# Kernel optimization log

Measured on AMD Instinct MI355X. Metric: run time of the kernel, lower is better.

## Reference

```python
import jax, jax.numpy as jnp
import numpy as np
import math

N_HEAD = 16
ROPE_BASE = 10000.0


def _rope_cos_sin(seq_len, head_dim, dtype):
    # standard RoPE tables: freqs_i = base^(-2i/d), i in [0, d/2)
    half = head_dim // 2
    inv_freq = ROPE_BASE ** (-(jnp.arange(half, dtype=jnp.float32) * 2.0 / head_dim))
    t = jnp.arange(seq_len, dtype=jnp.float32)
    ang = t[:, None] * inv_freq[None, :]  # [S, d/2]
    return jnp.cos(ang).astype(dtype), jnp.sin(ang).astype(dtype)


def _apply_rope(x, cos, sin):
    # x: [B, S, H, d]; rotate interleaved even/odd pairs
    x1 = x[..., 0::2]
    x2 = x[..., 1::2]
    c = cos[None, :, None, :]
    s = sin[None, :, None, :]
    out = jnp.stack([x1 * c - x2 * s, x1 * s + x2 * c], axis=-1)
    return out.reshape(x.shape)


def setup_inputs() -> dict:
    key = jax.random.key(0)
    kx, kq, kk, kv, ko = jax.random.split(key, 5)
    B, S, H = 2, 2048, 1024
    x = jax.random.normal(kx, (B, S, H), dtype=jnp.float32)
    scale = 0.02
    w_q = jax.random.normal(kq, (H, H), dtype=jnp.float32) * scale
    w_k = jax.random.normal(kk, (H, H), dtype=jnp.float32) * scale
    w_v = jax.random.normal(kv, (H, H), dtype=jnp.float32) * scale
    w_o = jax.random.normal(ko, (H, H), dtype=jnp.float32) * scale
    return {"x": x, "w_q": w_q, "w_k": w_k, "w_v": w_v, "w_o": w_o}


def reference(x, w_q, w_k, w_v, w_o):
    B, S, H = x.shape
    d = H // N_HEAD
    # torch nn.Linear(bias=False): y = x @ W^T, W is [out, in]
    q = (x @ w_q.T).reshape(B, S, N_HEAD, d)
    k = (x @ w_k.T).reshape(B, S, N_HEAD, d)
    v = (x @ w_v.T).reshape(B, S, N_HEAD, d)
    cos, sin = _rope_cos_sin(S, d, x.dtype)
    q = _apply_rope(q, cos, sin)
    k = _apply_rope(k, cos, sin)
    scores = jnp.einsum("bqhd,bkhd->bhqk", q, k) / math.sqrt(d)
    coefs = jax.nn.softmax(scores, axis=-1)
    # NOTE: causal mask is applied AFTER softmax via tril (no renormalization)
    causal = jnp.tril(jnp.ones((S, S), dtype=bool))
    coefs = jnp.where(causal[None, None], coefs, 0.0)
    out = jnp.einsum("bhqk,bkhd->bqhd", coefs, v).reshape(B, S, H)
    return out @ w_o.T
```

## Files before the change

kernel.cpp:

```cpp
#include <hip/hip_runtime.h>
#include <math.h>

#define SEQ   2048
#define HDIM  1024
#define NH    16
#define DH    64
#define MTOT  4096
#define BHTOT 32

typedef _Float16 half_t;
typedef __attribute__((ext_vector_type(2))) __fp16 fp16x2;
typedef __attribute__((ext_vector_type(4))) _Float16 half4;
typedef __attribute__((ext_vector_type(8))) _Float16 half8;
typedef __attribute__((ext_vector_type(4))) float float4v;

typedef __attribute__((address_space(1))) const unsigned int guint;
typedef __attribute__((address_space(3))) unsigned int luint;
__device__ __forceinline__ void glds16(const half_t* g, half_t* l) {
    __builtin_amdgcn_global_load_lds((guint*)g, (luint*)l, 16, 0, 0);
}

__global__ __launch_bounds__(256)
void prep(const float* __restrict__ x,  const float* __restrict__ wq,
          const float* __restrict__ wk, const float* __restrict__ wv,
          const float* __restrict__ wo,
          half_t* __restrict__ xh,  half_t* __restrict__ wqh,
          half_t* __restrict__ wkh, half_t* __restrict__ wvh,
          half_t* __restrict__ woh, float2* __restrict__ rope)
{
    const int bid = blockIdx.x;
    if (bid < 8192) {
        int i = bid * 256 + threadIdx.x;
        const float* s; half_t* d;
        if (i < 1048576) { s = x; d = xh; }
        else {
            int j = i - 1048576;
            int w = j >> 18; i = j & 262143;
            s = (w == 0) ? wq : (w == 1) ? wk : (w == 2) ? wv : wo;
            d = (w == 0) ? wqh : (w == 1) ? wkh : (w == 2) ? wvh : woh;
        }
        float4 v = ((const float4*)s)[i];
        union { half_t h[4]; uint2 u; } tmp;
        tmp.h[0] = (half_t)v.x; tmp.h[1] = (half_t)v.y;
        tmp.h[2] = (half_t)v.z; tmp.h[3] = (half_t)v.w;
        ((uint2*)d)[i] = tmp.u;
    } else {
        int tt = (bid - 8192) * 256 + threadIdx.x;
        int s = tt >> 5, j = tt & 31;
        float inv = powf(10000.0f, -(float)j / 32.0f);
        float ang = (float)s * inv;
        rope[tt] = make_float2(cosf(ang), sinf(ang));
    }
}

__global__ __launch_bounds__(256, 5)
void gemm_qkv(const half_t* __restrict__ A,
              const half_t* __restrict__ w0, const half_t* __restrict__ w1,
              const half_t* __restrict__ w2,
              half_t* __restrict__ Qb, half_t* __restrict__ Kb,
              half_t* __restrict__ Vtb,
              const float2* __restrict__ rope)
{
    const int mode = blockIdx.z;
    const half_t* Bw = (mode == 1) ? w1 : (mode == 2) ? w2 : w0;

    __shared__ __align__(16) half_t Tsh[2][128][64];
    half_t (*Ash)[64] = Tsh[0];
    half_t (*Bsh)[64] = Tsh[1];

    const int t    = threadIdx.x;
    const int lane = t & 63;
    const int wave = t >> 6;
    const int quad = lane >> 4;
    const int l16  = lane & 15;
    const int wr   = (wave >> 1) * 64;
    const int wc   = (wave & 1) * 64;
    const int bm   = blockIdx.x, bn = blockIdx.y;

    const int srow   = lane >> 3;
    const int schunk = (lane & 7) ^ (srow & 3);
    const half_t* Asrc = A  + (size_t)(bm * 128 + srow) * HDIM + schunk * 8;
    const half_t* Bsrc = Bw + (size_t)(bn * 128 + srow) * HDIM + schunk * 8;
    const int swz = (l16 & 3) << 4;

    float4v acc[4][4] = {};

    for (int kt = 0; kt < HDIM / 64; ++kt) {
        const half_t* Ak = Asrc + kt * 64;
        const half_t* Bk = Bsrc + kt * 64;
#pragma unroll
        for (int c = 0; c < 4; ++c) {
            const int r8 = wave * 32 + c * 8;
            glds16(Ak + (size_t)r8 * HDIM, &Ash[r8][0]);
            glds16(Bk + (size_t)r8 * HDIM, &Bsh[r8][0]);
        }
        __syncthreads();
#pragma unroll
        for (int kk = 0; kk < 2; ++kk) {
            const int cb = ((quad << 4) | (kk << 6)) ^ swz;
            half8 af[4], bf[4];
#pragma unroll
            for (int mb = 0; mb < 4; ++mb)
                af[mb] = *(const half8*)((const char*)&Ash[wr + mb * 16 + l16][0] + cb);
#pragma unroll
            for (int nb = 0; nb < 4; ++nb)
                bf[nb] = *(const half8*)((const char*)&Bsh[wc + nb * 16 + l16][0] + cb);
#pragma unroll
            for (int mb = 0; mb < 4; ++mb)
#pragma unroll
                for (int nb = 0; nb < 4; ++nb)
                    acc[mb][nb] = __builtin_amdgcn_mfma_f32_16x16x32_f16(af[mb], bf[nb], acc[mb][nb], 0, 0, 0);
        }
        __syncthreads();
    }

    if (mode == 2) {
#pragma unroll
        for (int mb = 0; mb < 4; ++mb)
#pragma unroll
            for (int nb = 0; nb < 4; ++nb) {
                int row0 = bm * 128 + wr + mb * 16 + quad * 4;
                int col  = bn * 128 + wc + nb * 16 + l16;
                int b = row0 >> 11, s0 = row0 & 2047;
                int h = col >> 6,  dd = col & 63;
                union { half_t h4[4]; uint2 u; } tmp;
#pragma unroll
                for (int r = 0; r < 4; ++r) tmp.h4[r] = (half_t)acc[mb][nb][r];
                *(uint2*)&Vtb[((size_t)((b * NH + h) * DH + dd)) * SEQ + s0] = tmp.u;
            }
        return;
    }
    {
        half_t* Ob = (mode == 0) ? Qb : Kb;
        const float scl = (mode == 0) ? 0.125f * 1.44269504088896f : 1.0f;
        const int h = (bn * 128 + wc) >> 6;
        float* E = (float*)&Tsh[0][0][0] + wave * 1088;
#pragma unroll
        for (int mb = 0; mb < 4; ++mb) {
#pragma unroll
            for (int nb = 0; nb < 4; ++nb)
#pragma unroll
                for (int r = 0; r < 4; ++r)
                    E[(quad * 4 + r) * 68 + nb * 16 + l16] = acc[mb][nb][r];
            __asm__ volatile("s_waitcnt lgkmcnt(0)" ::: "memory");
#pragma unroll
            for (int c = 0; c < 2; ++c) {
                const int uidx = c * 64 + lane;
                const int row = uidx >> 3, ch = uidx & 7;
                const int sg = bm * 128 + wr + mb * 16 + row;
                const int b = sg >> 11, s = sg & 2047;
                const float* Er = E + row * 68 + ch * 8;
                const float4 e0 = *(const float4*)Er;
                const float4 e1 = *(const float4*)(Er + 4);
                const float4* rp = (const float4*)(rope + (size_t)s * 32 + ch * 4);
                const float4 r01 = rp[0];
                const float4 r23 = rp[1];
                union { half_t hh[8]; uint4 u; } o;
                o.hh[0] = (half_t)((e0.x * r01.x - e0.y * r01.y) * scl);
                o.hh[1] = (half_t)((e0.x * r01.y + e0.y * r01.x) * scl);
                o.hh[2] = (half_t)((e0.z * r01.z - e0.w * r01.w) * scl);
                o.hh[3] = (half_t)((e0.z * r01.w + e0.w * r01.z) * scl);
                o.hh[4] = (half_t)((e1.x * r23.x - e1.y * r23.y) * scl);
                o.hh[5] = (half_t)((e1.x * r23.y + e1.y * r23.x) * scl);
                o.hh[6] = (half_t)((e1.z * r23.z - e1.w * r23.w) * scl);
                o.hh[7] = (half_t)((e1.z * r23.w + e1.w * r23.z) * scl);
                *(uint4*)&Ob[((size_t)((b * NH + h) * SEQ + s)) * DH + ch * 8] = o.u;
            }
        }
    }
}

__global__ __launch_bounds__(256)
void gemm_out(const half_t* __restrict__ A, const half_t* __restrict__ W,
              float* __restrict__ outF)
{
    __shared__ __align__(16) half_t Ash[2][64][64];
    __shared__ __align__(16) half_t Bsh[2][64][64];

    const int t    = threadIdx.x;
    const int lane = t & 63;
    const int wave = t >> 6;
    const int quad = lane >> 4;
    const int l16  = lane & 15;
    const int wr   = (wave >> 1) * 32;
    const int wc   = (wave & 1) * 32;
    const int bm   = blockIdx.x, bn = blockIdx.y;

    const int srow   = lane >> 3;
    const int schunk = (lane & 7) ^ (srow & 3);
    const half_t* Asrc = A + (size_t)(bm * 64 + srow) * HDIM + schunk * 8;
    const half_t* Bsrc = W + (size_t)(bn * 64 + srow) * HDIM + schunk * 8;
    const int swz = (l16 & 3) << 4;

    auto stage = [&](int kt, int buf) {
        const half_t* Ak = Asrc + kt * 64;
        const half_t* Bk = Bsrc + kt * 64;
#pragma unroll
        for (int c = 0; c < 2; ++c) {
            const int r8 = wave * 16 + c * 8;
            glds16(Ak + (size_t)r8 * HDIM, &Ash[buf][r8][0]);
            glds16(Bk + (size_t)r8 * HDIM, &Bsh[buf][r8][0]);
        }
    };

    float4v acc[2][2] = {};

    stage(0, 0);
    __asm__ volatile("s_waitcnt vmcnt(0)" ::: "memory");
    __builtin_amdgcn_s_barrier();
    __builtin_amdgcn_sched_barrier(0);

    for (int kt = 0; kt < HDIM / 64; ++kt) {
        const int cur = kt & 1, nxt = cur ^ 1;
        if (kt + 1 < HDIM / 64) stage(kt + 1, nxt);
#pragma unroll
        for (int kk = 0; kk < 2; ++kk) {
            const int cb = ((quad << 4) | (kk << 6)) ^ swz;
            half8 af[2], bf[2];
#pragma unroll
            for (int mb = 0; mb < 2; ++mb)
                af[mb] = *(const half8*)((const char*)&Ash[cur][wr + mb * 16 + l16][0] + cb);
#pragma unroll
            for (int nb = 0; nb < 2; ++nb)
                bf[nb] = *(const half8*)((const char*)&Bsh[cur][wc + nb * 16 + l16][0] + cb);
#pragma unroll
            for (int mb = 0; mb < 2; ++mb)
#pragma unroll
                for (int nb = 0; nb < 2; ++nb)
                    acc[mb][nb] = __builtin_amdgcn_mfma_f32_16x16x32_f16(af[mb], bf[nb], acc[mb][nb], 0, 0, 0);
        }
        __asm__ volatile("s_waitcnt vmcnt(0)" ::: "memory");
        __builtin_amdgcn_s_barrier();
        __builtin_amdgcn_sched_barrier(0);
    }

#pragma unroll
    for (int mb = 0; mb < 2; ++mb)
#pragma unroll
        for (int nb = 0; nb < 2; ++nb) {
            int row0 = bm * 64 + wr + mb * 16 + quad * 4;
            int col  = bn * 64 + wc + nb * 16 + l16;
#pragma unroll
            for (int r = 0; r < 4; ++r)
                outF[(size_t)(row0 + r) * HDIM + col] = acc[mb][nb][r];
        }
}

__global__ __launch_bounds__(512, 4)
void attn_fused(const half_t* __restrict__ Qb, const half_t* __restrict__ Kb,
                const half_t* __restrict__ Vtb, half_t* __restrict__ AOut)
{
    const int bx = blockIdx.x;
    const int p  = bx >> 1;
    const int hf = bx & 1;
    const int bh = blockIdx.y;
    const int NT = SEQ / 128;

    __shared__ __align__(16) half_t Ksh[2][128][64];
    __shared__ __align__(16) half_t Vsh[2][64][128];

    const int t = threadIdx.x;
    const int wave = t >> 6, lane = t & 63, quad = lane >> 4, l16 = lane & 15;
    const int heavy = wave >> 2, wl = wave & 3;
    const int qtile = heavy ? (15 - p) : p;
    const int q0 = qtile * 128 + hf * 64 + wl * 16;
    const int vtop = 15 - p;

    const half_t* Qp = Qb + ((size_t)bh * SEQ + q0 + l16) * DH + quad * 8;
    const half8 qf0 = *(const half8*)Qp;
    const half8 qf1 = *(const half8*)(Qp + 32);

    float4v o[4] = {};
    float4v ls = {};

    const int krow = lane >> 3, kpos = lane & 7;
    const int kchunk = kpos ^ krow;
    const half_t* Ksrc = Kb + ((size_t)bh * SEQ + wave * 16 + krow) * DH + kchunk * 8;
    const int ko1 = ((quad ^ (l16 & 7)) * 8);
    const int ko2 = ko1 ^ 32;

    const int sr  = t >> 3;
    const int sc0 = t & 7;
    const half_t* Vg = Vtb + ((size_t)bh * DH + sr) * SEQ + sc0 * 8;
    const int vso0 = ((sc0    ) ^ (sr & 15)) * 8;
    const int vso1 = ((sc0 + 8) ^ (sr & 15)) * 8;

    {
        uint4 va0 = *(const uint4*)(Vg);
        uint4 va1 = *(const uint4*)(Vg + 64);
        glds16(Ksrc,          &Ksh[0][wave * 16][0]);
        glds16(Ksrc + 8 * DH, &Ksh[0][wave * 16 + 8][0]);
        *(uint4*)&Vsh[0][sr][vso0] = va0;
        *(uint4*)&Vsh[0][sr][vso1] = va1;
    }
    __asm__ volatile("s_waitcnt vmcnt(0)" ::: "memory");
    __asm__ volatile("s_waitcnt lgkmcnt(0)" ::: "memory");
    __builtin_amdgcn_s_barrier();
    __builtin_amdgcn_sched_barrier(0);

    for (int T = 0; T < NT; ++T) {
        const int cur = T & 1, nxt = cur ^ 1;
        const bool kn = (T + 1 < NT);
        const bool vn = kn && (T + 1 <= vtop);

        uint4 va0, va1;
        if (vn) {
            va0 = *(const uint4*)(Vg + (T + 1) * 128);
            va1 = *(const uint4*)(Vg + (T + 1) * 128 + 64);
        }
        if (kn) {
            const half_t* Kn = Ksrc + (size_t)(T + 1) * 128 * DH;
            glds16(Kn,          &Ksh[nxt][wave * 16][0]);
            glds16(Kn + 8 * DH, &Ksh[nxt][wave * 16 + 8][0]);
        }

#pragma unroll
        for (int hh = 0; hh < 2; ++hh) {
            float4v sc[4];
            __builtin_amdgcn_s_setprio(1);
#pragma unroll
            for (int nb = 0; nb < 4; ++nb) {
                const half_t* kp = &Ksh[cur][hh * 64 + nb * 16 + l16][0];
                half8 kf0 = *(const half8*)(kp + ko1);
                half8 kf1 = *(const half8*)(kp + ko2);
                float4v a = {};
                a = __builtin_amdgcn_mfma_f32_16x16x32_f16(kf0, qf0, a, 0, 0, 0);
                a = __builtin_amdgcn_mfma_f32_16x16x32_f16(kf1, qf1, a, 0, 0, 0);
                sc[nb] = a;
            }
            __builtin_amdgcn_s_setprio(0);

#pragma unroll
            for (int nb = 0; nb < 4; ++nb)
#pragma unroll
                for (int r = 0; r < 4; ++r) {
                    float e = __builtin_amdgcn_exp2f(sc[nb][r]);
                    sc[nb][r] = e;
                    ls[r] += e;
                }

            const int kbase = T * 128 + hh * 64;
            if (kbase <= q0 + 15) {
                if (kbase + 63 > q0) {
                    int qg = q0 + l16;
#pragma unroll
                    for (int nb = 0; nb < 4; ++nb)
#pragma unroll
                        for (int r = 0; r < 4; ++r)
                            if (kbase + nb * 16 + quad * 4 + r > qg) sc[nb][r] = 0.f;
                }
                half4 pf[4];
#pragma unroll
                for (int nb = 0; nb < 4; ++nb) {
                    union { fp16x2 v2[2]; half4 v4; } u;
                    u.v2[0] = __builtin_amdgcn_cvt_pkrtz(sc[nb][0], sc[nb][1]);
                    u.v2[1] = __builtin_amdgcn_cvt_pkrtz(sc[nb][2], sc[nb][3]);
                    pf[nb] = u.v4;
                }
                __builtin_amdgcn_s_setprio(1);
#pragma unroll
                for (int md = 0; md < 4; ++md) {
                    const char* vrow = (const char*)&Vsh[cur][md * 16 + l16][0];
#pragma unroll
                    for (int nb = 0; nb < 4; ++nb) {
                        const int chunk = (hh * 8 + nb * 2 + (quad >> 1)) ^ l16;
                        half4 vf = *(const half4*)(vrow + chunk * 16 + (quad & 1) * 8);
                        o[md] = __builtin_amdgcn_mfma_f32_16x16x16f16(vf, pf[nb], o[md], 0, 0, 0);
                    }
                }
                __builtin_amdgcn_s_setprio(0);
            }
        }

        if (vn) {
            *(uint4*)&Vsh[nxt][sr][vso0] = va0;
            *(uint4*)&Vsh[nxt][sr][vso1] = va1;
        }
        __asm__ volatile("s_waitcnt vmcnt(0)" ::: "memory");
        __asm__ volatile("s_waitcnt lgkmcnt(0)" ::: "memory");
        __builtin_amdgcn_s_barrier();
        __builtin_amdgcn_sched_barrier(0);
    }

    const int b = bh >> 4, h = bh & 15;
    const int orow = lane >> 2, occ = (lane & 3) * 16;
    half_t* scr = (heavy ? (half_t*)Vsh : (half_t*)Ksh) + wl * 1152;
    half_t (*Osh)[72] = (half_t(*)[72])scr;
    {
        float rs = (ls[0] + ls[1]) + (ls[2] + ls[3]);
        rs += __shfl_xor(rs, 16, 64);
        rs += __shfl_xor(rs, 32, 64);
        const float inv = 1.0f / rs;
#pragma unroll
        for (int md = 0; md < 4; ++md)
#pragma unroll
            for (int r = 0; r < 4; ++r)
                Osh[l16][md * 16 + quad * 4 + r] = (half_t)(o[md][r] * inv);
        __asm__ volatile("s_waitcnt lgkmcnt(0)" ::: "memory");
        uint4 o0 = *(const uint4*)&Osh[orow][occ];
        uint4 o1 = *(const uint4*)&Osh[orow][occ + 8];
        const int s = q0 + orow;
        half_t* dst = AOut + ((size_t)(b * SEQ + s)) * HDIM + h * DH + occ;
        *(uint4*)dst       = o0;
        *(uint4*)(dst + 8) = o1;
    }
}

extern "C" void kernel_launch(void* const* d_in, const int* in_sizes, int n_in,
                              void* d_out, int out_size, void* d_ws, size_t ws_size,
                              hipStream_t stream)
{
    const float* x  = (const float*)d_in[0];
    const float* wq = (const float*)d_in[1];
    const float* wk = (const float*)d_in[2];
    const float* wv = (const float*)d_in[3];
    const float* wo = (const float*)d_in[4];
    float* out = (float*)d_out;

    char* ws = (char*)d_ws;
    size_t off = 0;
    auto alloc = [&](size_t bytes) -> void* {
        void* p = ws + off;
        off += (bytes + 255) & ~(size_t)255;
        return p;
    };
    half_t* xh   = (half_t*)alloc((size_t)MTOT * HDIM * 2);
    half_t* wqh  = (half_t*)alloc((size_t)HDIM * HDIM * 2);
    half_t* wkh  = (half_t*)alloc((size_t)HDIM * HDIM * 2);
    half_t* wvh  = (half_t*)alloc((size_t)HDIM * HDIM * 2);
    half_t* woh  = (half_t*)alloc((size_t)HDIM * HDIM * 2);
    half_t* Qb   = (half_t*)alloc((size_t)BHTOT * SEQ * DH * 2);
    half_t* Kb   = (half_t*)alloc((size_t)BHTOT * SEQ * DH * 2);
    half_t* Vtb  = (half_t*)alloc((size_t)BHTOT * SEQ * DH * 2);
    half_t* ah   = (half_t*)alloc((size_t)MTOT * HDIM * 2);
    float2* rope = (float2*)alloc((size_t)SEQ * 32 * sizeof(float2));

    prep<<<8448, 256, 0, stream>>>(x, wq, wk, wv, wo, xh, wqh, wkh, wvh, woh, rope);

    gemm_qkv<<<dim3(32, 8, 3), 256, 0, stream>>>(xh, wqh, wkh, wvh,
                                                 Qb, Kb, Vtb, rope);
    attn_fused<<<dim3(16, 32), 512, 0, stream>>>(Qb, Kb, Vtb, ah);
    gemm_out<<<dim3(64, 16), 256, 0, stream>>>(ah, woh, out);
}
```

Measured before the change: 186.6 us.

## Process paired light and heavy query tiles per wave to reuse K/V fragments

Each wave now handles two 16-row query groups (one from tile p and one from tile 15-p) instead of one, so every K and V fragment read from shared memory feeds two MFMA chains. The grid is halved to 8x32 blocks with each block covering a full 128-row tile pair, and the launch bounds drop to 2 blocks per SM to leave room for the doubled accumulators. The aim is to cut LDS traffic per MFMA and raise the share of time spent on matrix math. In exchange, register pressure roughly doubles and occupancy and the number of blocks fall, which could hurt latency hiding. The block-to-head mapping is also reordered.

```diff
diff --git a/kernel.cpp b/kernel.cpp
--- a/kernel.cpp
+++ b/kernel.cpp
@@ -246,14 +246,12 @@
         }
 }
 
-__global__ __launch_bounds__(512, 4)
+__global__ __launch_bounds__(512, 2)
 void attn_fused(const half_t* __restrict__ Qb, const half_t* __restrict__ Kb,
                 const half_t* __restrict__ Vtb, half_t* __restrict__ AOut)
 {
-    const int bx = blockIdx.x;
-    const int p  = bx >> 1;
-    const int hf = bx & 1;
-    const int bh = blockIdx.y;
+    const int p  = blockIdx.y >> 2;
+    const int bh = (blockIdx.y & 3) * 8 + blockIdx.x;
     const int NT = SEQ / 128;
 
     __shared__ __align__(16) half_t Ksh[2][128][64];
@@ -261,17 +259,19 @@
 
     const int t = threadIdx.x;
     const int wave = t >> 6, lane = t & 63, quad = lane >> 4, l16 = lane & 15;
-    const int heavy = wave >> 2, wl = wave & 3;
-    const int qtile = heavy ? (15 - p) : p;
-    const int q0 = qtile * 128 + hf * 64 + wl * 16;
+    const int q0g[2] = { p * 128 + wave * 16, (15 - p) * 128 + wave * 16 };
     const int vtop = 15 - p;
 
-    const half_t* Qp = Qb + ((size_t)bh * SEQ + q0 + l16) * DH + quad * 8;
-    const half8 qf0 = *(const half8*)Qp;
-    const half8 qf1 = *(const half8*)(Qp + 32);
-
-    float4v o[4] = {};
-    float4v ls = {};
+    half8 qf0[2], qf1[2];
+#pragma unroll
+    for (int g = 0; g < 2; ++g) {
+        const half_t* Qp = Qb + ((size_t)bh * SEQ + q0g[g] + l16) * DH + quad * 8;
+        qf0[g] = *(const half8*)Qp;
+        qf1[g] = *(const half8*)(Qp + 32);
+    }
+
+    float4v o0[4] = {}, o1[4] = {};
+    float4v ls0 = {}, ls1 = {};
 
     const int krow = lane >> 3, kpos = lane & 7;
     const int kchunk = kpos ^ krow;
@@ -316,7 +316,7 @@
 
 #pragma unroll
         for (int hh = 0; hh < 2; ++hh) {
-            float4v sc[4];
+            float4v s0[4], s1[4];
             __builtin_amdgcn_s_setprio(1);
 #pragma unroll
             for (int nb = 0; nb < 4; ++nb) {
@@ -324,9 +324,13 @@
                 half8 kf0 = *(const half8*)(kp + ko1);
                 half8 kf1 = *(const half8*)(kp + ko2);
                 float4v a = {};
-                a = __builtin_amdgcn_mfma_f32_16x16x32_f16(kf0, qf0, a, 0, 0, 0);
-                a = __builtin_amdgcn_mfma_f32_16x16x32_f16(kf1, qf1, a, 0, 0, 0);
-                sc[nb] = a;
+                a = __builtin_amdgcn_mfma_f32_16x16x32_f16(kf0, qf0[0], a, 0, 0, 0);
+                a = __builtin_amdgcn_mfma_f32_16x16x32_f16(kf1, qf1[0], a, 0, 0, 0);
+                s0[nb] = a;
+                float4v b = {};
+                b = __builtin_amdgcn_mfma_f32_16x16x32_f16(kf0, qf0[1], b, 0, 0, 0);
+                b = __builtin_amdgcn_mfma_f32_16x16x32_f16(kf1, qf1[1], b, 0, 0, 0);
+                s1[nb] = b;
             }
             __builtin_amdgcn_s_setprio(0);
 
@@ -334,38 +338,72 @@
             for (int nb = 0; nb < 4; ++nb)
 #pragma unroll
                 for (int r = 0; r < 4; ++r) {
-                    float e = __builtin_amdgcn_exp2f(sc[nb][r]);
-                    sc[nb][r] = e;
-                    ls[r] += e;
+                    float e0 = __builtin_amdgcn_exp2f(s0[nb][r]);
+                    float e1 = __builtin_amdgcn_exp2f(s1[nb][r]);
+                    s0[nb][r] = e0; ls0[r] += e0;
+                    s1[nb][r] = e1; ls1[r] += e1;
                 }
 
             const int kbase = T * 128 + hh * 64;
-            if (kbase <= q0 + 15) {
-                if (kbase + 63 > q0) {
-                    int qg = q0 + l16;
+            const bool act0 = (kbase <= q0g[0] + 15);
+            const bool act1 = (kbase <= q0g[1] + 15);
+            if (act1) {
+                if (kbase + 63 > q0g[1]) {
+                    int qg = q0g[1] + l16;
 #pragma unroll
                     for (int nb = 0; nb < 4; ++nb)
 #pragma unroll
                         for (int r = 0; r < 4; ++r)
-                            if (kbase + nb * 16 + quad * 4 + r > qg) sc[nb][r] = 0.f;
-                }
-                half4 pf[4];
+                            if (kbase + nb * 16 + quad * 4 + r > qg) s1[nb][r] = 0.f;
+                }
+                if (act0 && kbase + 63 > q0g[0]) {
+                    int qg = q0g[0] + l16;
+#pragma unroll
+                    for (int nb = 0; nb < 4; ++nb)
+#pragma unroll
+                        for (int r = 0; r < 4; ++r)
+                            if (kbase + nb * 16 + quad * 4 + r > qg) s0[nb][r] = 0.f;
+                }
+                half4 pf1[4], pf0[4];
 #pragma unroll
                 for (int nb = 0; nb < 4; ++nb) {
                     union { fp16x2 v2[2]; half4 v4; } u;
-                    u.v2[0] = __builtin_amdgcn_cvt_pkrtz(sc[nb][0], sc[nb][1]);
-                    u.v2[1] = __builtin_amdgcn_cvt_pkrtz(sc[nb][2], sc[nb][3]);
-                    pf[nb] = u.v4;
+                    u.v2[0] = __builtin_amdgcn_cvt_pkrtz(s1[nb][0], s1[nb][1]);
+                    u.v2[1] = __builtin_amdgcn_cvt_pkrtz(s1[nb][2], s1[nb][3]);
+                    pf1[nb] = u.v4;
+                }
+                if (act0) {
+#pragma unroll
+                    for (int nb = 0; nb < 4; ++nb) {
+                        union { fp16x2 v2[2]; half4 v4; } u;
+                        u.v2[0] = __builtin_amdgcn_cvt_pkrtz(s0[nb][0], s0[nb][1]);
+                        u.v2[1] = __builtin_amdgcn_cvt_pkrtz(s0[nb][2], s0[nb][3]);
+                        pf0[nb] = u.v4;
+                    }
                 }
                 __builtin_amdgcn_s_setprio(1);
-#pragma unroll
-                for (int md = 0; md < 4; ++md) {
-                    const char* vrow = (const char*)&Vsh[cur][md * 16 + l16][0];
-#pragma unroll
-                    for (int nb = 0; nb < 4; ++nb) {
-                        const int chunk = (hh * 8 + nb * 2 + (quad >> 1)) ^ l16;
-                        half4 vf = *(const half4*)(vrow + chunk * 16 + (quad & 1) * 8);
-                        o[md] = __builtin_amdgcn_mfma_f32_16x16x16f16(vf, pf[nb], o[md], 0, 0, 0);
+                if (act0) {
+#pragma unroll
+                    for (int md = 0; md < 4; ++md) {
+                        const char* vrow = (const char*)&Vsh[cur][md * 16 + l16][0];
+#pragma unroll
+                        for (int nb = 0; nb < 4; ++nb) {
+                            const int chunk = (hh * 8 + nb * 2 + (quad >> 1)) ^ l16;
+                            half4 vf = *(const half4*)(vrow + chunk * 16 + (quad & 1) * 8);
+                            o1[md] = __builtin_amdgcn_mfma_f32_16x16x16f16(vf, pf1[nb], o1[md], 0, 0, 0);
+                            o0[md] = __builtin_amdgcn_mfma_f32_16x16x16f16(vf, pf0[nb], o0[md], 0, 0, 0);
+                        }
+                    }
+                } else {
+#pragma unroll
+                    for (int md = 0; md < 4; ++md) {
+                        const char* vrow = (const char*)&Vsh[cur][md * 16 + l16][0];
+#pragma unroll
+                        for (int nb = 0; nb < 4; ++nb) {
+                            const int chunk = (hh * 8 + nb * 2 + (quad >> 1)) ^ l16;
+                            half4 vf = *(const half4*)(vrow + chunk * 16 + (quad & 1) * 8);
+                            o1[md] = __builtin_amdgcn_mfma_f32_16x16x16f16(vf, pf1[nb], o1[md], 0, 0, 0);
+                        }
                     }
                 }
                 __builtin_amdgcn_s_setprio(0);
@@ -384,10 +422,12 @@
 
     const int b = bh >> 4, h = bh & 15;
     const int orow = lane >> 2, occ = (lane & 3) * 16;
-    half_t* scr = (heavy ? (half_t*)Vsh : (half_t*)Ksh) + wl * 1152;
+    half_t* scr = (half_t*)Ksh + wave * 1152;
     half_t (*Osh)[72] = (half_t(*)[72])scr;
-    {
-        float rs = (ls[0] + ls[1]) + (ls[2] + ls[3]);
+#pragma unroll
+    for (int g = 0; g < 2; ++g) {
+        const float4v& lsg = g ? ls1 : ls0;
+        float rs = (lsg[0] + lsg[1]) + (lsg[2] + lsg[3]);
         rs += __shfl_xor(rs, 16, 64);
         rs += __shfl_xor(rs, 32, 64);
         const float inv = 1.0f / rs;
@@ -395,14 +435,15 @@
         for (int md = 0; md < 4; ++md)
 #pragma unroll
             for (int r = 0; r < 4; ++r)
-                Osh[l16][md * 16 + quad * 4 + r] = (half_t)(o[md][r] * inv);
+                Osh[l16][md * 16 + quad * 4 + r] =
+                    (half_t)(((g ? o1 : o0)[md][r]) * inv);
         __asm__ volatile("s_waitcnt lgkmcnt(0)" ::: "memory");
-        uint4 o0 = *(const uint4*)&Osh[orow][occ];
-        uint4 o1 = *(const uint4*)&Osh[orow][occ + 8];
-        const int s = q0 + orow;
+        uint4 v0 = *(const uint4*)&Osh[orow][occ];
+        uint4 v1 = *(const uint4*)&Osh[orow][occ + 8];
+        const int s = q0g[g] + orow;
         half_t* dst = AOut + ((size_t)(b * SEQ + s)) * HDIM + h * DH + occ;
-        *(uint4*)dst       = o0;
-        *(uint4*)(dst + 8) = o1;
+        *(uint4*)dst       = v0;
+        *(uint4*)(dst + 8) = v1;
     }
 }
 
@@ -439,6 +480,6 @@
 
     gemm_qkv<<<dim3(32, 8, 3), 256, 0, stream>>>(xh, wqh, wkh, wvh,
                                                  Qb, Kb, Vtb, rope);
-    attn_fused<<<dim3(16, 32), 512, 0, stream>>>(Qb, Kb, Vtb, ah);
+    attn_fused<<<dim3(8, 32), 512, 0, stream>>>(Qb, Kb, Vtb, ah);
     gemm_out<<<dim3(64, 16), 256, 0, stream>>>(ah, woh, out);
 }
```

After: 186.2 us. About the same (-0.2%).

## Double-buffer QKV GEMM shared-memory tiles with K-step of 32

Applied to the files above, without the earlier changes.

Restructures the QKV projection GEMM main loop to use two shared-memory buffers with a K-tile of 32 instead of one buffer with a K-tile of 64. The next tile's global-to-LDS loads are issued before the MFMAs on the current tile, so load latency can overlap with compute. Each iteration now ends with a single wait-and-barrier instead of two syncthreads. Total LDS use stays the same, but there are twice as many iterations, each doing less MFMA work per barrier.

```diff
diff --git a/kernel.cpp b/kernel.cpp
--- a/kernel.cpp
+++ b/kernel.cpp
@@ -64,9 +64,7 @@
     const int mode = blockIdx.z;
     const half_t* Bw = (mode == 1) ? w1 : (mode == 2) ? w2 : w0;
 
-    __shared__ __align__(16) half_t Tsh[2][128][64];
-    half_t (*Ash)[64] = Tsh[0];
-    half_t (*Bsh)[64] = Tsh[1];
+    __shared__ __align__(16) half_t Tsh[2][2][128][32];
 
     const int t    = threadIdx.x;
     const int lane = t & 63;
@@ -77,41 +75,47 @@
     const int wc   = (wave & 1) * 64;
     const int bm   = blockIdx.x, bn = blockIdx.y;
 
-    const int srow   = lane >> 3;
-    const int schunk = (lane & 7) ^ (srow & 3);
+    const int srow   = lane >> 2;
+    const int schunk = (lane & 3) ^ (srow & 3);
     const half_t* Asrc = A  + (size_t)(bm * 128 + srow) * HDIM + schunk * 8;
     const half_t* Bsrc = Bw + (size_t)(bn * 128 + srow) * HDIM + schunk * 8;
     const int swz = (l16 & 3) << 4;
 
+    auto stage = [&](int kt, int buf) {
+        const half_t* Ak = Asrc + kt * 32;
+        const half_t* Bk = Bsrc + kt * 32;
+        glds16(Ak + (size_t)(wave * 32)      * HDIM, &Tsh[buf][0][wave * 32][0]);
+        glds16(Ak + (size_t)(wave * 32 + 16) * HDIM, &Tsh[buf][0][wave * 32 + 16][0]);
+        glds16(Bk + (size_t)(wave * 32)      * HDIM, &Tsh[buf][1][wave * 32][0]);
+        glds16(Bk + (size_t)(wave * 32 + 16) * HDIM, &Tsh[buf][1][wave * 32 + 16][0]);
+    };
+
     float4v acc[4][4] = {};
 
-    for (int kt = 0; kt < HDIM / 64; ++kt) {
-        const half_t* Ak = Asrc + kt * 64;
-        const half_t* Bk = Bsrc + kt * 64;
-#pragma unroll
-        for (int c = 0; c < 4; ++c) {
-            const int r8 = wave * 32 + c * 8;
-            glds16(Ak + (size_t)r8 * HDIM, &Ash[r8][0]);
-            glds16(Bk + (size_t)r8 * HDIM, &Bsh[r8][0]);
-        }
-        __syncthreads();
-#pragma unroll
-        for (int kk = 0; kk < 2; ++kk) {
-            const int cb = ((quad << 4) | (kk << 6)) ^ swz;
-            half8 af[4], bf[4];
-#pragma unroll
-            for (int mb = 0; mb < 4; ++mb)
-                af[mb] = *(const half8*)((const char*)&Ash[wr + mb * 16 + l16][0] + cb);
+    stage(0, 0);
+    __asm__ volatile("s_waitcnt vmcnt(0)" ::: "memory");
+    __builtin_amdgcn_s_barrier();
+    __builtin_amdgcn_sched_barrier(0);
+
+    for (int kt = 0; kt < HDIM / 32; ++kt) {
+        const int cur = kt & 1, nxt = cur ^ 1;
+        if (kt + 1 < HDIM / 32) stage(kt + 1, nxt);
+        const int cb = (quad << 4) ^ swz;
+        half8 af[4], bf[4];
+#pragma unroll
+        for (int mb = 0; mb < 4; ++mb)
+            af[mb] = *(const half8*)((const char*)&Tsh[cur][0][wr + mb * 16 + l16][0] + cb);
+#pragma unroll
+        for (int nb = 0; nb < 4; ++nb)
+            bf[nb] = *(const half8*)((const char*)&Tsh[cur][1][wc + nb * 16 + l16][0] + cb);
+#pragma unroll
+        for (int mb = 0; mb < 4; ++mb)
 #pragma unroll
             for (int nb = 0; nb < 4; ++nb)
-                bf[nb] = *(const half8*)((const char*)&Bsh[wc + nb * 16 + l16][0] + cb);
-#pragma unroll
-            for (int mb = 0; mb < 4; ++mb)
-#pragma unroll
-                for (int nb = 0; nb < 4; ++nb)
-                    acc[mb][nb] = __builtin_amdgcn_mfma_f32_16x16x32_f16(af[mb], bf[nb], acc[mb][nb], 0, 0, 0);
-        }
-        __syncthreads();
+                acc[mb][nb] = __builtin_amdgcn_mfma_f32_16x16x32_f16(af[mb], bf[nb], acc[mb][nb], 0, 0, 0);
+        __asm__ volatile("s_waitcnt vmcnt(0)" ::: "memory");
+        __builtin_amdgcn_s_barrier();
+        __builtin_amdgcn_sched_barrier(0);
     }
 
     if (mode == 2) {
@@ -134,7 +138,7 @@
         half_t* Ob = (mode == 0) ? Qb : Kb;
         const float scl = (mode == 0) ? 0.125f * 1.44269504088896f : 1.0f;
         const int h = (bn * 128 + wc) >> 6;
-        float* E = (float*)&Tsh[0][0][0] + wave * 1088;
+        float* E = (float*)&Tsh[0][0][0][0] + wave * 1088;
 #pragma unroll
         for (int mb = 0; mb < 4; ++mb) {
 #pragma unroll
```

After: 180.5 us. -3.3%, faster.
